# Kernel optimization log

Measured on AMD Instinct MI355X. Metric: run time of the kernel, lower is better.

The kernel has to match this reference:

```python
import jax, jax.numpy as jnp
import numpy as np

N = 100000        # number of nodes
E = 3200000       # number of edges (avg degree 32)
D_IN = 128
D_OUT = 128


def setup_inputs() -> dict:
    key = jax.random.key(0)
    k_x, k_src, k_dst, k_w, k_W, k_b = jax.random.split(key, 6)
    x = jax.random.normal(k_x, (N, D_IN), dtype=jnp.float32)
    edge_src = jax.random.randint(k_src, (E,), 0, N, dtype=jnp.int32)
    edge_dst = jnp.sort(jax.random.randint(k_dst, (E,), 0, N, dtype=jnp.int32))
    edge_weight = jax.random.uniform(k_w, (E,), dtype=jnp.float32)
    # Linear params, init uniform(-stdv, stdv) with stdv = 1/sqrt(in_features)
    stdv = 1.0 / np.sqrt(D_IN)
    W = jax.random.uniform(k_W, (D_IN, D_OUT), dtype=jnp.float32, minval=-stdv, maxval=stdv)
    b = jax.random.uniform(k_b, (D_OUT,), dtype=jnp.float32, minval=-stdv, maxval=stdv)
    return {"x": x, "W": W, "b": b, "edge_weight": edge_weight,
            "edge_src": edge_src, "edge_dst": edge_dst}


def reference(x, W, b, edge_weight, edge_src, edge_dst):
    # support = W(input)  -- dense projection [N, D_OUT]
    support = x @ W + b
    # output = spmm(adj, support): out[dst] += w_e * support[src]
    msgs = support[edge_src] * edge_weight[:, None]          # [E, D_OUT]
    out = jax.ops.segment_sum(msgs, edge_dst, num_segments=x.shape[0])
    return out
```

## Files before the change

kernel.cpp:

```cpp
#include <hip/hip_runtime.h>

#define D 128

typedef unsigned short u16;
typedef unsigned int   u32;
typedef __attribute__((ext_vector_type(8))) short bf16x8;
typedef __attribute__((ext_vector_type(4))) float f32x4;

__device__ __forceinline__ u16 f32_to_bf16(float f) {
    unsigned u = __float_as_uint(f);
    unsigned rounding = 0x7fffu + ((u >> 16) & 1u);
    return (u16)((u + rounding) >> 16);
}

__device__ __forceinline__ float bf16_to_f32(u16 s) {
    return __uint_as_float(((unsigned)s) << 16);
}

__global__ __launch_bounds__(256) void prep_kernel(
    const float* __restrict__ W, u16* __restrict__ Wt)
{
    int idx = blockIdx.x * 256 + threadIdx.x;
    int n = idx >> 7;
    int k = idx & 127;
    Wt[idx] = f32_to_bf16(W[k * 128 + n]);
}

__global__ __launch_bounds__(256) void gemm_mfma_kernel(
    const float* __restrict__ x, const u16* __restrict__ Wt,
    const float* __restrict__ b, u16* __restrict__ sup, int N)
{
    const int lane = threadIdx.x & 63;
    const int wave = threadIdx.x >> 6;
    const int col  = lane & 15;
    const int quad = lane >> 4;
    const int row0 = blockIdx.x * 64 + wave * 16;
    const int m    = row0 + col;
    const bool mvalid = (m < N);

    f32x4 acc[8];
    #pragma unroll
    for (int nt = 0; nt < 8; ++nt) {
        float bias = b[nt * 16 + col];
        acc[nt][0] = bias; acc[nt][1] = bias;
        acc[nt][2] = bias; acc[nt][3] = bias;
    }

    const float* xrow = x + (size_t)m * D;

    #pragma unroll
    for (int ks = 0; ks < 4; ++ks) {
        const int k0 = ks * 32 + quad * 8;

        float af[8];
        if (mvalid) {
            float4 v0 = *(const float4*)(xrow + k0);
            float4 v1 = *(const float4*)(xrow + k0 + 4);
            af[0] = v0.x; af[1] = v0.y; af[2] = v0.z; af[3] = v0.w;
            af[4] = v1.x; af[5] = v1.y; af[6] = v1.z; af[7] = v1.w;
        } else {
            #pragma unroll
            for (int j = 0; j < 8; ++j) af[j] = 0.f;
        }

        bf16x8 ahi, alo;
        #pragma unroll
        for (int j = 0; j < 8; ++j) {
            u16 h = f32_to_bf16(af[j]);
            float r = af[j] - bf16_to_f32(h);
            ahi[j] = (short)h;
            alo[j] = (short)f32_to_bf16(r);
        }

        #pragma unroll
        for (int nt = 0; nt < 8; ++nt) {
            bf16x8 bfrag = *(const bf16x8*)(Wt + (size_t)(nt * 16 + col) * D + k0);
            acc[nt] = __builtin_amdgcn_mfma_f32_16x16x32_bf16(alo, bfrag, acc[nt], 0, 0, 0);
            acc[nt] = __builtin_amdgcn_mfma_f32_16x16x32_bf16(ahi, bfrag, acc[nt], 0, 0, 0);
        }
    }

    #pragma unroll
    for (int reg = 0; reg < 4; ++reg) {
        int r = row0 + quad * 4 + reg;
        if (r < N) {
            #pragma unroll
            for (int nt = 0; nt < 8; ++nt) {
                sup[(size_t)r * D + nt * 16 + col] = f32_to_bf16(acc[nt][reg]);
            }
        }
    }
}

__global__ __launch_bounds__(256) void rowptr_kernel(
    const int* __restrict__ edst, int* __restrict__ rp, int E, int N)
{
    int e = blockIdx.x * 256 + threadIdx.x;
    if (e >= E) return;
    int d = edst[e];
    int prev = (e == 0) ? -1 : edst[e - 1];
    for (int n = prev + 1; n <= d; ++n) rp[n] = e;
    if (e == E - 1) {
        for (int n = d + 1; n <= N; ++n) rp[n] = E;
    }
}

__global__ __launch_bounds__(256) void spmm_kernel(
    const u16* __restrict__ sup, const float* __restrict__ ew,
    const int* __restrict__ esrc, const int* __restrict__ rp,
    float* __restrict__ out, int N)
{
    const int wave = threadIdx.x >> 6;
    const int lane = threadIdx.x & 63;
    const int node = blockIdx.x * 4 + wave;
    if (node >= N) return;

    const int start = __builtin_amdgcn_readfirstlane(rp[node]);
    const int end   = __builtin_amdgcn_readfirstlane(rp[node + 1]);

    float acc0 = 0.f;
    float acc1 = 0.f;

    for (int base = start; base < end; base += 64) {
        const int cnt = min(64, end - base);
        const int mi  = base + lane;
        int sv = 0;
        int wv = 0;
        if (mi < end) {
            sv = esrc[mi];
            wv = __float_as_int(ew[mi]);
        }

        for (int i0 = 0; i0 < cnt; i0 += 8) {
            u32 u[8];
            float wf[8];
            #pragma unroll
            for (int t = 0; t < 8; ++t) {
                int s  = __builtin_amdgcn_readlane(sv, i0 + t);
                int wb = __builtin_amdgcn_readlane(wv, i0 + t);
                const u32* prow = (const u32*)(sup + ((size_t)(u32)s << 7));
                u[t]  = prow[lane];
                wf[t] = __int_as_float(wb);
            }
            #pragma unroll
            for (int t = 0; t < 8; ++t) {
                acc0 = fmaf(wf[t], __uint_as_float(u[t] << 16),         acc0);
                acc1 = fmaf(wf[t], __uint_as_float(u[t] & 0xffff0000u), acc1);
            }
        }
    }

    float2 o = make_float2(acc0, acc1);
    *(float2*)(out + (size_t)node * D + lane * 2) = o;
}

extern "C" void kernel_launch(void* const* d_in, const int* in_sizes, int n_in,
                              void* d_out, int out_size, void* d_ws, size_t ws_size,
                              hipStream_t stream) {
    const float* x    = (const float*)d_in[0];
    const float* W    = (const float*)d_in[1];
    const float* b    = (const float*)d_in[2];
    const float* ew   = (const float*)d_in[3];
    const int*   esrc = (const int*)d_in[4];
    const int*   edst = (const int*)d_in[5];
    float* out = (float*)d_out;

    const int N = in_sizes[0] / D;
    const int E = in_sizes[3];

    u16* sup = (u16*)d_ws;
    int* rp  = (int*)((char*)d_ws + (size_t)N * D * sizeof(u16));
    u16* Wt  = (u16*)((char*)rp + ((size_t)N + 16) * sizeof(int));

    hipLaunchKernelGGL(prep_kernel, dim3(64), dim3(256), 0, stream, W, Wt);
    hipLaunchKernelGGL(gemm_mfma_kernel, dim3((N + 63) / 64), dim3(256), 0, stream,
                       x, Wt, b, sup, N);
    hipLaunchKernelGGL(rowptr_kernel, dim3((E + 255) / 256), dim3(256), 0, stream,
                       edst, rp, E, N);

    hipLaunchKernelGGL(spmm_kernel, dim3((N + 3) / 4), dim3(256), 0, stream,
                       sup, ew, esrc, rp, out, N);
}
```

Measured before the change: 270.1 us.

## Slice support into 16-column panels and split SpMM across feature slices

```diff
diff --git a/kernel.cpp b/kernel.cpp
--- a/kernel.cpp
+++ b/kernel.cpp
@@ -6,6 +6,7 @@
 typedef unsigned int   u32;
 typedef __attribute__((ext_vector_type(8))) short bf16x8;
 typedef __attribute__((ext_vector_type(4))) float f32x4;
+typedef __attribute__((ext_vector_type(2))) float f32x2;
 
 __device__ __forceinline__ u16 f32_to_bf16(float f) {
     unsigned u = __float_as_uint(f);
@@ -86,7 +87,7 @@
         if (r < N) {
             #pragma unroll
             for (int nt = 0; nt < 8; ++nt) {
-                sup[(size_t)r * D + nt * 16 + col] = f32_to_bf16(acc[nt][reg]);
+                sup[((size_t)nt * N + r) * 16 + col] = f32_to_bf16(acc[nt][reg]);
             }
         }
     }
@@ -110,48 +111,69 @@
     const int* __restrict__ esrc, const int* __restrict__ rp,
     float* __restrict__ out, int N)
 {
-    const int wave = threadIdx.x >> 6;
-    const int lane = threadIdx.x & 63;
-    const int node = blockIdx.x * 4 + wave;
+    const int b     = blockIdx.x;
+    const int slice = b & 7;
+    const int grp   = b >> 3;
+    const int wave  = threadIdx.x >> 6;
+    const int lane  = threadIdx.x & 63;
+    const int node  = grp * 4 + wave;
     if (node >= N) return;
+
+    const int eg = lane >> 3;
+    const int fo = lane & 7;
 
     const int start = __builtin_amdgcn_readfirstlane(rp[node]);
     const int end   = __builtin_amdgcn_readfirstlane(rp[node + 1]);
 
-    float acc0 = 0.f;
-    float acc1 = 0.f;
+    const u32* sbase = (const u32*)(sup + (size_t)slice * (size_t)N * 16);
+
+    float acc0 = 0.f, acc1 = 0.f;
 
     for (int base = start; base < end; base += 64) {
         const int cnt = min(64, end - base);
         const int mi  = base + lane;
-        int sv = 0;
-        int wv = 0;
+        int   sv = 0;
+        float wv = 0.f;
         if (mi < end) {
-            sv = esrc[mi];
-            wv = __float_as_int(ew[mi]);
-        }
-
-        for (int i0 = 0; i0 < cnt; i0 += 8) {
-            u32 u[8];
-            float wf[8];
-            #pragma unroll
-            for (int t = 0; t < 8; ++t) {
-                int s  = __builtin_amdgcn_readlane(sv, i0 + t);
-                int wb = __builtin_amdgcn_readlane(wv, i0 + t);
-                const u32* prow = (const u32*)(sup + ((size_t)(u32)s << 7));
-                u[t]  = prow[lane];
-                wf[t] = __int_as_float(wb);
-            }
-            #pragma unroll
-            for (int t = 0; t < 8; ++t) {
-                acc0 = fmaf(wf[t], __uint_as_float(u[t] << 16),         acc0);
-                acc1 = fmaf(wf[t], __uint_as_float(u[t] & 0xffff0000u), acc1);
-            }
-        }
-    }
-
-    float2 o = make_float2(acc0, acc1);
-    *(float2*)(out + (size_t)node * D + lane * 2) = o;
+            sv = __builtin_nontemporal_load(esrc + mi);
+            wv = __builtin_nontemporal_load(ew + mi);
+        }
+
+        for (int i0 = 0; i0 < cnt; i0 += 16) {
+            const int idxA = i0 + eg;
+            const int idxB = i0 + 8 + eg;
+            const int cA = (idxA < cnt) ? idxA : (cnt - 1);
+            const int cB = (idxB < cnt) ? idxB : (cnt - 1);
+            const int   sA = __shfl(sv, cA);
+            const int   sB = __shfl(sv, cB);
+            float wA = __shfl(wv, cA);
+            float wB = __shfl(wv, cB);
+            if (idxA >= cnt) wA = 0.f;
+            if (idxB >= cnt) wB = 0.f;
+
+            const u32 uA = sbase[(size_t)(u32)sA * 8 + fo];
+            const u32 uB = sbase[(size_t)(u32)sB * 8 + fo];
+
+            acc0 = fmaf(wA, __uint_as_float(uA << 16),         acc0);
+            acc1 = fmaf(wA, __uint_as_float(uA & 0xffff0000u), acc1);
+            acc0 = fmaf(wB, __uint_as_float(uB << 16),         acc0);
+            acc1 = fmaf(wB, __uint_as_float(uB & 0xffff0000u), acc1);
+        }
+    }
+
+    #pragma unroll
+    for (int m = 8; m <= 32; m <<= 1) {
+        acc0 += __shfl_xor(acc0, m);
+        acc1 += __shfl_xor(acc1, m);
+    }
+
+    if (eg == 0) {
+        f32x2 o;
+        o.x = acc0;
+        o.y = acc1;
+        f32x2* dst = (f32x2*)(out + (size_t)node * D + slice * 16 + fo * 2);
+        __builtin_nontemporal_store(o, dst);
+    }
 }
 
 extern "C" void kernel_launch(void* const* d_in, const int* in_sizes, int n_in,
@@ -178,6 +200,7 @@
     hipLaunchKernelGGL(rowptr_kernel, dim3((E + 255) / 256), dim3(256), 0, stream,
                        edst, rp, E, N);
 
-    hipLaunchKernelGGL(spmm_kernel, dim3((N + 3) / 4), dim3(256), 0, stream,
+    int grid_spmm = ((N + 3) / 4) * 8;
+    hipLaunchKernelGGL(spmm_kernel, dim3(grid_spmm), dim3(256), 0, stream,
                        sup, ew, esrc, rp, out, N);
 }
```

Result: slower. 445.1 us (+64.8%).
